# Kernel tuning notes

Hardware: AMD Instinct MI355X
Metric: run time of the kernel (lower is better)

The kernel has to match this reference:

```python
import jax, jax.numpy as jnp
import numpy as np

EMBED_DIM = 128
LAYER_NUM = 5
NUM_GRAPHS = 8192
ATOM_VOCAB = 119
BOND_VOCAB = 8  # get_bond_feature_int_dims()[0] + 3
BN_EPS = 1e-5


def setup_inputs() -> dict:
    key = jax.random.key(0)
    ks = jax.random.split(key, 12)
    N, E, d = 300000, 600000, EMBED_DIM
    x = jax.random.randint(ks[0], (N, 9), 0, ATOM_VOCAB)
    edge_index = jax.random.randint(ks[1], (2, E), 0, N)
    edge_attr = jax.random.randint(ks[2], (E, 3), 0, BOND_VOCAB)
    batch = jnp.sort(jax.random.randint(ks[3], (N,), 0, NUM_GRAPHS))
    s1 = (2.0 / (ATOM_VOCAB + d)) ** 0.5  # xavier-ish scales
    atom_emb = jax.random.normal(ks[4], (ATOM_VOCAB, d), jnp.float32) * s1
    bond_emb = jax.random.normal(ks[5], (BOND_VOCAB, d), jnp.float32) * s1
    L = LAYER_NUM
    W1 = jax.random.normal(ks[6], (L, d, 2 * d), jnp.float32) * (2.0 / (3 * d)) ** 0.5
    b1 = jnp.zeros((L, 2 * d), jnp.float32)
    W2 = jax.random.normal(ks[7], (L, 2 * d, d), jnp.float32) * (2.0 / (3 * d)) ** 0.5
    b2 = jnp.zeros((L, d), jnp.float32)
    gamma = jnp.ones((L, d), jnp.float32)
    beta = jnp.zeros((L, d), jnp.float32)
    return {"x": x, "edge_index": edge_index, "edge_attr": edge_attr, "batch": batch,
            "atom_emb": atom_emb, "bond_emb": bond_emb, "W1": W1, "b1": b1,
            "W2": W2, "b2": b2, "gamma": gamma, "beta": beta}


def reference(x, edge_index, edge_attr, batch, atom_emb, bond_emb, W1, b1, W2, b2, gamma, beta):
    # node / edge embeddings from first integer feature column
    h = atom_emb[x[:, 0]]                      # [N, d]
    e = bond_emb[edge_attr[:, 0]]              # [E, d]
    src, dst = edge_index[0], edge_index[1]
    N = h.shape[0]
    for l in range(LAYER_NUM):
        # GINE message: relu(h_src + edge_attr), scatter-sum to dst
        msg = jax.nn.relu(h[src] + e)                             # [E, d]
        agg = jax.ops.segment_sum(msg, dst, num_segments=N)       # [N, d]
        z = h + agg                                               # (1+eps)*h + agg, eps=0
        # GIN MLP: Linear(d,2d) -> ReLU -> Linear(2d,d)
        z = jax.nn.relu(z @ W1[l] + b1[l]) @ W2[l] + b2[l]
        # BatchNorm1d over nodes (training statistics, biased variance)
        mean = jnp.mean(z, axis=0)
        var = jnp.var(z, axis=0)
        z = (z - mean) * jax.lax.rsqrt(var + BN_EPS) * gamma[l] + beta[l]
        # dropout is identity in eval; relu except on last layer
        h = z if l == LAYER_NUM - 1 else jax.nn.relu(z)
    # global_add_pool
    return jax.ops.segment_sum(h, batch, num_segments=NUM_GRAPHS)  # [G, d]
```

## Files before the change

kernel.cpp:

```cpp
#include <hip/hip_runtime.h>
#include <hip/hip_bf16.h>

#define LAYERS 5
#define STATS_NB 16
#define EMAX 160

typedef __attribute__((ext_vector_type(8))) short short8v;
typedef __attribute__((ext_vector_type(4))) float f32x4;
typedef __attribute__((ext_vector_type(4))) unsigned int u32x4;

#define MFMA(a, b, c) __builtin_amdgcn_mfma_f32_16x16x32_bf16(a, b, c, 0, 0, 0)

__device__ __forceinline__ void atomAddF(float* p, float v) {
    __hip_atomic_fetch_add(p, v, __ATOMIC_RELAXED, __HIP_MEMORY_SCOPE_AGENT);
}

__device__ __forceinline__ float b2f(unsigned short u) { return __uint_as_float(((unsigned)u) << 16); }
__device__ __forceinline__ unsigned short f2b(float f) {
    __hip_bfloat16 h = __float2bfloat16(f);
    unsigned short u;
    __builtin_memcpy(&u, &h, 2);
    return u;
}
__device__ __forceinline__ void st4(unsigned short* p, float4 v) {
    ushort4 u;
    u.x = f2b(v.x); u.y = f2b(v.y); u.z = f2b(v.z); u.w = f2b(v.w);
    *(ushort4*)p = u;
}
__device__ __forceinline__ void unpack8(u32x4 u, float* f) {
#pragma unroll
    for (int k = 0; k < 4; ++k) {
        unsigned int w = u[k];
        f[2 * k]     = __uint_as_float(w << 16);
        f[2 * k + 1] = __uint_as_float(w & 0xffff0000u);
    }
}

__global__ void init_h_kernel(const int* __restrict__ x, const float* __restrict__ atom_emb,
                              unsigned short* __restrict__ h, float* __restrict__ scv,
                              float* __restrict__ shv, int N) {
    if (blockIdx.x == 0 && threadIdx.x < 128) {
        scv[threadIdx.x] = 1.f;
        shv[threadIdx.x] = 0.f;
    }
    int tid = blockIdx.x * blockDim.x + threadIdx.x;
    if (tid >= N * 32) return;
    int i = tid >> 5;
    int c4 = (tid & 31) << 2;
    int a = x[i * 9];
    float4 v = *(const float4*)(atom_emb + a * 128 + c4);
    st4(h + (size_t)i * 128 + c4, v);
}

__global__ void hist_kernel(const int* __restrict__ ei, int* __restrict__ cnt, int E) {
    int e = blockIdx.x * blockDim.x + threadIdx.x;
    if (e < E) atomicAdd(&cnt[ei[E + e]], 1);
}

__global__ void scan_block_sum(const int* __restrict__ cnt, int* __restrict__ bsum, int N) {
    __shared__ int ls[256];
    int base = blockIdx.x * 1024;
    int tid = threadIdx.x;
    int s = 0;
#pragma unroll
    for (int j = 0; j < 4; ++j) {
        int i = base + tid * 4 + j;
        if (i < N) s += cnt[i];
    }
    ls[tid] = s;
    __syncthreads();
    for (int off = 128; off > 0; off >>= 1) {
        if (tid < off) ls[tid] += ls[tid + off];
        __syncthreads();
    }
    if (tid == 0) bsum[blockIdx.x] = ls[0];
}

__global__ void scan_bsums(int* __restrict__ bsum, int nb) {
    if (blockIdx.x == 0 && threadIdx.x == 0) {
        int acc = 0;
        for (int i = 0; i < nb; ++i) { int v = bsum[i]; bsum[i] = acc; acc += v; }
    }
}

__global__ void scan_write(int* __restrict__ cnt_cursor, const int* __restrict__ bsum,
                           int* __restrict__ rowptr, int N, int E) {
    __shared__ int ls[256];
    int base = blockIdx.x * 1024;
    int tid = threadIdx.x;
    int v[4];
    int s = 0;
#pragma unroll
    for (int j = 0; j < 4; ++j) {
        int i = base + tid * 4 + j;
        v[j] = (i < N) ? cnt_cursor[i] : 0;
        s += v[j];
    }
    ls[tid] = s;
    __syncthreads();
    if (tid == 0) {
        int acc = 0;
        for (int i = 0; i < 256; ++i) { int t = ls[i]; ls[i] = acc; acc += t; }
    }
    __syncthreads();
    int off = bsum[blockIdx.x] + ls[tid];
#pragma unroll
    for (int j = 0; j < 4; ++j) {
        int i = base + tid * 4 + j;
        if (i < N) {
            rowptr[i] = off;
            cnt_cursor[i] = off;
            off += v[j];
        }
    }
    if (blockIdx.x == 0 && tid == 0) rowptr[N] = E;
}

__global__ void scatter_kernel(const int* __restrict__ ei, const int* __restrict__ eattr,
                               int* __restrict__ cursor, int* __restrict__ ebuf, int E) {
    int e = blockIdx.x * blockDim.x + threadIdx.x;
    if (e >= E) return;
    int d = ei[E + e];
    int pos = atomicAdd(&cursor[d], 1);
    ebuf[pos] = ei[e] | (eattr[e * 3] << 19);
}

__global__ void pack_w1_kernel(const float* __restrict__ W1,
                               unsigned short* __restrict__ wh, unsigned short* __restrict__ wl) {
    int tid = blockIdx.x * blockDim.x + threadIdx.x;
    if (tid >= LAYERS * 16 * 4 * 64) return;
    int lane = tid & 63;
    int ks = (tid >> 6) & 3;
    int nt = (tid >> 8) & 15;
    int l  = tid >> 12;
    int n  = nt * 16 + (lane & 15);
    int k0 = ks * 32 + ((lane >> 4) << 3);
    unsigned short hh[8], ll[8];
#pragma unroll
    for (int j = 0; j < 8; ++j) {
        float v = W1[((size_t)l * 128 + k0 + j) * 256 + n];
        hh[j] = f2b(v);
        ll[j] = f2b(v - b2f(hh[j]));
    }
    size_t off = (size_t)tid * 8;
    *(ushort4*)(wh + off)     = make_ushort4(hh[0], hh[1], hh[2], hh[3]);
    *(ushort4*)(wh + off + 4) = make_ushort4(hh[4], hh[5], hh[6], hh[7]);
    *(ushort4*)(wl + off)     = make_ushort4(ll[0], ll[1], ll[2], ll[3]);
    *(ushort4*)(wl + off + 4) = make_ushort4(ll[4], ll[5], ll[6], ll[7]);
}

__global__ void pack_w2_kernel(const float* __restrict__ W2,
                               unsigned short* __restrict__ wh, unsigned short* __restrict__ wl) {
    int tid = blockIdx.x * blockDim.x + threadIdx.x;
    if (tid >= LAYERS * 8 * 8 * 64) return;
    int lane = tid & 63;
    int ks = (tid >> 6) & 7;
    int nt = (tid >> 9) & 7;
    int l  = tid >> 12;
    int n  = nt * 16 + (lane & 15);
    int k0 = ks * 32 + ((lane >> 4) << 3);
    unsigned short hh[8], ll[8];
#pragma unroll
    for (int j = 0; j < 8; ++j) {
        float v = W2[((size_t)l * 256 + k0 + j) * 128 + n];
        hh[j] = f2b(v);
        ll[j] = f2b(v - b2f(hh[j]));
    }
    size_t off = (size_t)tid * 8;
    *(ushort4*)(wh + off)     = make_ushort4(hh[0], hh[1], hh[2], hh[3]);
    *(ushort4*)(wh + off + 4) = make_ushort4(hh[4], hh[5], hh[6], hh[7]);
    *(ushort4*)(wl + off)     = make_ushort4(ll[0], ll[1], ll[2], ll[3]);
    *(ushort4*)(wl + off + 4) = make_ushort4(ll[4], ll[5], ll[6], ll[7]);
}

__global__ __launch_bounds__(512, 6) void fused_mlp_kernel(
        const unsigned short* __restrict__ zin,
        const int* __restrict__ rowptr, const int* __restrict__ ebuf,
        const float* __restrict__ bond_emb,
        const float* __restrict__ scv, const float* __restrict__ shv, float clampv,
        const unsigned short* __restrict__ w1h, const unsigned short* __restrict__ w1l,
        const unsigned short* __restrict__ w2h, const unsigned short* __restrict__ w2l,
        const float* __restrict__ b1, const float* __restrict__ b2,
        unsigned short* __restrict__ zout, float* __restrict__ stats_part, int N) {
    __shared__ float bemb[8 * 128];
    __shared__ float scl[128], shl[128];
    __shared__ int els[EMAX];
    __shared__ int rp[65];
    __shared__ unsigned short xs[64][136];
    __shared__ unsigned short ts[64][136];

    int tid = threadIdx.x;
    int rowBase = blockIdx.x * 64;
    int lane = tid & 63;
    int wv = tid >> 6;

    for (int i = tid; i < 1024; i += 512) bemb[i] = bond_emb[i];
    if (tid < 128) { scl[tid] = scv[tid]; shl[tid] = shv[tid]; }
    if (tid >= 128 && tid <= 192) {
        int t = tid - 128;
        int rr = rowBase + t;
        rp[t] = rowptr[rr < N ? rr : N];
    }
    __syncthreads();
    int beg = rp[0];
    int cnt = rp[64] - beg;
    for (int i = tid; i < cnt && i < EMAX; i += 512) els[i] = ebuf[beg + i];
    __syncthreads();

    {
        int r = tid >> 3;
        int c0 = (tid & 7) << 4;
        int row = rowBase + r;
        float xv[16];
        if (row < N) {
            const unsigned short* hp = zin + (size_t)row * 128 + c0;
            u32x4 u0 = *(const u32x4*)hp;
            u32x4 u1 = *(const u32x4*)(hp + 8);
            float rv[16];
            unpack8(u0, rv);
            unpack8(u1, rv + 8);
#pragma unroll
            for (int i2 = 0; i2 < 16; ++i2)
                xv[i2] = fmaxf(fmaf(rv[i2], scl[c0 + i2], shl[c0 + i2]), clampv);
            int rb = rp[r] - beg;
            int re = rp[r + 1] - beg;
            const float* bemb_c = bemb + c0;
            for (int j = rb; j < re; ++j) {
                int ee = (j < EMAX) ? els[j] : ebuf[beg + j];
                int src = ee & 0x7FFFF;
                int b = ee >> 19;
                const unsigned short* sp = zin + (size_t)src * 128 + c0;
                u32x4 s0 = *(const u32x4*)sp;
                u32x4 s1 = *(const u32x4*)(sp + 8);
                float sv[16];
                unpack8(s0, sv);
                unpack8(s1, sv + 8);
                const float* bp = bemb_c + b * 128;
#pragma unroll
                for (int i2 = 0; i2 < 16; ++i2) {
                    float hv = fmaxf(fmaf(sv[i2], scl[c0 + i2], shl[c0 + i2]), clampv);
                    xv[i2] += fmaxf(hv + bp[i2], 0.f);
                }
            }
        } else {
#pragma unroll
            for (int i2 = 0; i2 < 16; ++i2) xv[i2] = 0.f;
        }
#pragma unroll
        for (int k = 0; k < 4; ++k) {
            *(ushort4*)(&xs[r][c0 + k * 4]) = make_ushort4(
                f2b(xv[k * 4 + 0]), f2b(xv[k * 4 + 1]), f2b(xv[k * 4 + 2]), f2b(xv[k * 4 + 3]));
        }
    }
    __syncthreads();

    int lrow = lane & 15;
    int lk8 = (lane >> 4) << 3;
    int rgrp = (lane >> 4) << 2;
    int wm = wv >> 2;
    int wn = wv & 3;

    f32x4 acc2[2][2];
#pragma unroll
    for (int mt = 0; mt < 2; ++mt)
#pragma unroll
        for (int t = 0; t < 2; ++t) acc2[mt][t] = (f32x4){0.f, 0.f, 0.f, 0.f};

#pragma unroll
    for (int half = 0; half < 2; ++half) {
        f32x4 acc1[2][2];
#pragma unroll
        for (int mt = 0; mt < 2; ++mt)
#pragma unroll
            for (int t = 0; t < 2; ++t) acc1[mt][t] = (f32x4){0.f, 0.f, 0.f, 0.f};

#pragma unroll
        for (int ks = 0; ks < 4; ++ks) {
            int kb = ks * 32 + lk8;
            short8v ah[2];
#pragma unroll
            for (int mt = 0; mt < 2; ++mt) {
                int mrow = (wm * 2 + mt) * 16 + lrow;
                ah[mt] = *(const short8v*)(&xs[mrow][kb]);
            }
#pragma unroll
            for (int t = 0; t < 2; ++t) {
                int nt = half * 8 + wn * 2 + t;
                size_t off = ((size_t)(nt * 4 + ks) * 64 + lane) * 8;
                short8v wh = *(const short8v*)(w1h + off);
                short8v wl = *(const short8v*)(w1l + off);
#pragma unroll
                for (int mt = 0; mt < 2; ++mt) {
                    acc1[mt][t] = MFMA(ah[mt], wl, acc1[mt][t]);
                    acc1[mt][t] = MFMA(ah[mt], wh, acc1[mt][t]);
                }
            }
        }

        if (half) __syncthreads();

#pragma unroll
        for (int t = 0; t < 2; ++t) {
            int coll = (wn * 2 + t) * 16 + lrow;
            float bb = b1[half * 128 + coll];
#pragma unroll
            for (int mt = 0; mt < 2; ++mt) {
                int row0 = (wm * 2 + mt) * 16 + rgrp;
#pragma unroll
                for (int r = 0; r < 4; ++r) {
                    ts[row0 + r][coll] = f2b(fmaxf(acc1[mt][t][r] + bb, 0.f));
                }
            }
        }
        __syncthreads();

#pragma unroll
        for (int ksl = 0; ksl < 4; ++ksl) {
            int kb = ksl * 32 + lk8;
            short8v ah[2];
#pragma unroll
            for (int mt = 0; mt < 2; ++mt) {
                int mrow = (wm * 2 + mt) * 16 + lrow;
                ah[mt] = *(const short8v*)(&ts[mrow][kb]);
            }
#pragma unroll
            for (int t = 0; t < 2; ++t) {
                int nt = wn * 2 + t;
                int ks = half * 4 + ksl;
                size_t off = ((size_t)(nt * 8 + ks) * 64 + lane) * 8;
                short8v wh = *(const short8v*)(w2h + off);
                short8v wl = *(const short8v*)(w2l + off);
#pragma unroll
                for (int mt = 0; mt < 2; ++mt) {
                    acc2[mt][t] = MFMA(ah[mt], wl, acc2[mt][t]);
                    acc2[mt][t] = MFMA(ah[mt], wh, acc2[mt][t]);
                }
            }
        }
    }

#pragma unroll
    for (int t = 0; t < 2; ++t) {
        int col = (wn * 2 + t) * 16 + lrow;
        float bb = b2[col];
        float s = 0.f, q = 0.f;
#pragma unroll
        for (int mt = 0; mt < 2; ++mt) {
#pragma unroll
            for (int r = 0; r < 4; ++r) {
                int row = rowBase + (wm * 2 + mt) * 16 + rgrp + r;
                if (row < N) {
                    float zv = acc2[mt][t][r] + bb;
                    zout[(size_t)row * 128 + col] = f2b(zv);
                    s += zv;
                    q += zv * zv;
                }
            }
        }
        s += __shfl_xor(s, 16, 64);
        s += __shfl_xor(s, 32, 64);
        q += __shfl_xor(q, 16, 64);
        q += __shfl_xor(q, 32, 64);
        if (lane < 16) {
            float* sp = stats_part + (size_t)(blockIdx.x & (STATS_NB - 1)) * 256;
            atomAddF(sp + col, s);
            atomAddF(sp + 128 + col, q);
        }
    }
}

__global__ void reduce_stats_sc_kernel(float* __restrict__ part,
                                       const float* __restrict__ gamma, const float* __restrict__ beta,
                                       float* __restrict__ scv, float* __restrict__ shv, float invN) {
    __shared__ float ls[256];
    int c = threadIdx.x;
    float s = 0.f;
    for (int i = 0; i < STATS_NB; ++i) {
        s += part[i * 256 + c];
        part[i * 256 + c] = 0.f;
    }
    ls[c] = s;
    __syncthreads();
    if (c < 128) {
        float mean = ls[c] * invN;
        float var = ls[128 + c] * invN - mean * mean;
        float sc = rsqrtf(var + 1e-5f) * gamma[c];
        scv[c] = sc;
        shv[c] = beta[c] - mean * sc;
    }
}

__global__ __launch_bounds__(256) void pool_seg_kernel(const unsigned short* __restrict__ zb,
                                                       const int* __restrict__ batch,
                                                       const float* __restrict__ scv,
                                                       const float* __restrict__ shv,
                                                       float* __restrict__ out, int N, int G) {
    int g = blockIdx.x * 4 + (threadIdx.x >> 6);
    if (g >= G) return;
    int lane = threadIdx.x & 63;
    int lo = 0, hi = N;
    while (lo < hi) { int m = (lo + hi) >> 1; if (batch[m] < g) lo = m + 1; else hi = m; }
    int s = lo;
    hi = N;
    while (lo < hi) { int m = (lo + hi) >> 1; if (batch[m] < g + 1) lo = m + 1; else hi = m; }
    int e = lo;
    int c2 = lane * 2;
    float a0 = 0.f, a1 = 0.f;
    for (int i = s; i < e; ++i) {
        ushort2 u = *(const ushort2*)(zb + (size_t)i * 128 + c2);
        a0 += b2f(u.x);
        a1 += b2f(u.y);
    }
    float cntf = (float)(e - s);
    float o0 = scv[c2] * a0 + cntf * shv[c2];
    float o1 = scv[c2 + 1] * a1 + cntf * shv[c2 + 1];
    *(float2*)(out + (size_t)g * 128 + c2) = make_float2(o0, o1);
}

extern "C" void kernel_launch(void* const* d_in, const int* in_sizes, int n_in,
                              void* d_out, int out_size, void* d_ws, size_t ws_size,
                              hipStream_t stream) {
    const int* x        = (const int*)d_in[0];
    const int* ei       = (const int*)d_in[1];
    const int* eattr    = (const int*)d_in[2];
    const int* batch    = (const int*)d_in[3];
    const float* atom_e = (const float*)d_in[4];
    const float* bond_e = (const float*)d_in[5];
    const float* W1     = (const float*)d_in[6];
    const float* b1     = (const float*)d_in[7];
    const float* W2     = (const float*)d_in[8];
    const float* b2     = (const float*)d_in[9];
    const float* gamma  = (const float*)d_in[10];
    const float* beta   = (const float*)d_in[11];

    int N = in_sizes[0] / 9;
    int E = in_sizes[1] / 2;
    int G = out_size / 128;

    auto align = [](size_t v) { return (v + 255) & ~(size_t)255; };
    char* ws = (char*)d_ws;
    unsigned short* bufA = (unsigned short*)ws; ws += align((size_t)N * 128 * 2);
    unsigned short* bufB = (unsigned short*)ws; ws += align((size_t)N * 128 * 2);
    int* rowptr  = (int*)ws;                 ws += align((size_t)(N + 1) * 4);
    int* cursor  = (int*)ws;                 ws += align((size_t)N * 4);
    int* ebuf    = (int*)ws;                 ws += align((size_t)E * 4);
    int* bsum    = (int*)ws;                 ws += align((size_t)4096 * 4);
    unsigned short* w1h = (unsigned short*)ws; ws += align((size_t)LAYERS * 32768 * 2);
    unsigned short* w1l = (unsigned short*)ws; ws += align((size_t)LAYERS * 32768 * 2);
    unsigned short* w2h = (unsigned short*)ws; ws += align((size_t)LAYERS * 32768 * 2);
    unsigned short* w2l = (unsigned short*)ws; ws += align((size_t)LAYERS * 32768 * 2);
    float* stats_part = (float*)ws;          ws += align((size_t)STATS_NB * 256 * 4);
    float* scv = (float*)ws;                 ws += align(128 * 4);
    float* shv = (float*)ws;

    float invN = 1.0f / (float)N;
    int nf4 = N * 32;
    int nb = (N + 1023) / 1024;

    init_h_kernel<<<(nf4 + 255) / 256, 256, 0, stream>>>(x, atom_e, bufA, scv, shv, N);

    hipMemsetAsync(cursor, 0, (size_t)N * 4, stream);
    hist_kernel<<<(E + 255) / 256, 256, 0, stream>>>(ei, cursor, E);
    scan_block_sum<<<nb, 256, 0, stream>>>(cursor, bsum, N);
    scan_bsums<<<1, 64, 0, stream>>>(bsum, nb);
    scan_write<<<nb, 256, 0, stream>>>(cursor, bsum, rowptr, N, E);
    scatter_kernel<<<(E + 255) / 256, 256, 0, stream>>>(ei, eattr, cursor, ebuf, E);

    pack_w1_kernel<<<(LAYERS * 16 * 4 * 64 + 255) / 256, 256, 0, stream>>>(W1, w1h, w1l);
    pack_w2_kernel<<<(LAYERS * 8 * 8 * 64 + 255) / 256, 256, 0, stream>>>(W2, w2h, w2l);
    hipMemsetAsync(stats_part, 0, (size_t)STATS_NB * 256 * 4, stream);

    unsigned short* zin = bufA;
    unsigned short* zout = bufB;
    for (int l = 0; l < LAYERS; ++l) {
        float clampv = (l == 0) ? -3.0e38f : 0.0f;
        fused_mlp_kernel<<<(N + 63) / 64, 512, 0, stream>>>(
            zin, rowptr, ebuf, bond_e, scv, shv, clampv,
            w1h + (size_t)l * 32768, w1l + (size_t)l * 32768,
            w2h + (size_t)l * 32768, w2l + (size_t)l * 32768,
            b1 + (size_t)l * 256, b2 + (size_t)l * 128,
            zout, stats_part, N);
        reduce_stats_sc_kernel<<<1, 256, 0, stream>>>(stats_part, gamma + (size_t)l * 128,
                                                      beta + (size_t)l * 128, scv, shv, invN);
        unsigned short* tmp = zin; zin = zout; zout = tmp;
    }

    pool_seg_kernel<<<(G + 3) / 4, 256, 0, stream>>>(zin, batch, scv, shv, (float*)d_out, N, G);
}
```

Baseline: 866.7 us.

## Switch MLP to 32x32 MFMA tiles and fold BN stats reduction into consumers

Replaces the 16x16x32 bf16 MFMA tiling with 32x32x16 MFMAs, with each wave computing a single 32x32 tile. The weight packing kernels are rewritten to the new fragment layout. The separate single-block reduce_stats kernel is removed: each layer's kernel and the pool kernel now sum the previous layer's partial statistics and compute scale/shift themselves, using per-layer stats buffers that are zeroed once. This removes five tiny serial launches at the cost of redundant per-block reduction work and a different MFMA register and LDS access pattern.

```diff
diff --git a/kernel.cpp b/kernel.cpp
--- a/kernel.cpp
+++ b/kernel.cpp
@@ -6,10 +6,10 @@
 #define EMAX 160
 
 typedef __attribute__((ext_vector_type(8))) short short8v;
-typedef __attribute__((ext_vector_type(4))) float f32x4;
+typedef __attribute__((ext_vector_type(16))) float f32x16;
 typedef __attribute__((ext_vector_type(4))) unsigned int u32x4;
 
-#define MFMA(a, b, c) __builtin_amdgcn_mfma_f32_16x16x32_bf16(a, b, c, 0, 0, 0)
+#define MFMA32(a, b, c) __builtin_amdgcn_mfma_f32_32x32x16_bf16(a, b, c, 0, 0, 0)
 
 __device__ __forceinline__ void atomAddF(float* p, float v) {
     __hip_atomic_fetch_add(p, v, __ATOMIC_RELAXED, __HIP_MEMORY_SCOPE_AGENT);
@@ -37,12 +37,7 @@
 }
 
 __global__ void init_h_kernel(const int* __restrict__ x, const float* __restrict__ atom_emb,
-                              unsigned short* __restrict__ h, float* __restrict__ scv,
-                              float* __restrict__ shv, int N) {
-    if (blockIdx.x == 0 && threadIdx.x < 128) {
-        scv[threadIdx.x] = 1.f;
-        shv[threadIdx.x] = 0.f;
-    }
+                              unsigned short* __restrict__ h, int N) {
     int tid = blockIdx.x * blockDim.x + threadIdx.x;
     if (tid >= N * 32) return;
     int i = tid >> 5;
@@ -128,13 +123,13 @@
 __global__ void pack_w1_kernel(const float* __restrict__ W1,
                                unsigned short* __restrict__ wh, unsigned short* __restrict__ wl) {
     int tid = blockIdx.x * blockDim.x + threadIdx.x;
-    if (tid >= LAYERS * 16 * 4 * 64) return;
+    if (tid >= LAYERS * 8 * 8 * 64) return;
     int lane = tid & 63;
-    int ks = (tid >> 6) & 3;
-    int nt = (tid >> 8) & 15;
+    int ks = (tid >> 6) & 7;
+    int nt = (tid >> 9) & 7;
     int l  = tid >> 12;
-    int n  = nt * 16 + (lane & 15);
-    int k0 = ks * 32 + ((lane >> 4) << 3);
+    int n  = nt * 32 + (lane & 31);
+    int k0 = ks * 16 + ((lane >> 5) << 3);
     unsigned short hh[8], ll[8];
 #pragma unroll
     for (int j = 0; j < 8; ++j) {
@@ -152,13 +147,13 @@
 __global__ void pack_w2_kernel(const float* __restrict__ W2,
                                unsigned short* __restrict__ wh, unsigned short* __restrict__ wl) {
     int tid = blockIdx.x * blockDim.x + threadIdx.x;
-    if (tid >= LAYERS * 8 * 8 * 64) return;
+    if (tid >= LAYERS * 4 * 16 * 64) return;
     int lane = tid & 63;
-    int ks = (tid >> 6) & 7;
-    int nt = (tid >> 9) & 7;
+    int ks = (tid >> 6) & 15;
+    int nt = (tid >> 10) & 3;
     int l  = tid >> 12;
-    int n  = nt * 16 + (lane & 15);
-    int k0 = ks * 32 + ((lane >> 4) << 3);
+    int n  = nt * 32 + (lane & 31);
+    int k0 = ks * 16 + ((lane >> 5) << 3);
     unsigned short hh[8], ll[8];
 #pragma unroll
     for (int j = 0; j < 8; ++j) {
@@ -173,15 +168,18 @@
     *(ushort4*)(wl + off + 4) = make_ushort4(ll[4], ll[5], ll[6], ll[7]);
 }
 
+template <bool FIRST>
 __global__ __launch_bounds__(512, 6) void fused_mlp_kernel(
         const unsigned short* __restrict__ zin,
         const int* __restrict__ rowptr, const int* __restrict__ ebuf,
         const float* __restrict__ bond_emb,
-        const float* __restrict__ scv, const float* __restrict__ shv, float clampv,
+        const float* __restrict__ stats_prev,
+        const float* __restrict__ gamma_prev, const float* __restrict__ beta_prev,
+        float invN, float clampv,
         const unsigned short* __restrict__ w1h, const unsigned short* __restrict__ w1l,
         const unsigned short* __restrict__ w2h, const unsigned short* __restrict__ w2l,
         const float* __restrict__ b1, const float* __restrict__ b2,
-        unsigned short* __restrict__ zout, float* __restrict__ stats_part, int N) {
+        unsigned short* __restrict__ zout, float* __restrict__ stats_out, int N) {
     __shared__ float bemb[8 * 128];
     __shared__ float scl[128], shl[128];
     __shared__ int els[EMAX];
@@ -195,9 +193,18 @@
     int wv = tid >> 6;
 
     for (int i = tid; i < 1024; i += 512) bemb[i] = bond_emb[i];
-    if (tid < 128) { scl[tid] = scv[tid]; shl[tid] = shv[tid]; }
-    if (tid >= 128 && tid <= 192) {
-        int t = tid - 128;
+    if (FIRST) {
+        if (tid < 128) { scl[tid] = 1.f; shl[tid] = 0.f; }
+    } else {
+        if (tid < 256) {
+            float s = 0.f;
+#pragma unroll
+            for (int i = 0; i < STATS_NB; ++i) s += stats_prev[i * 256 + tid];
+            if (tid < 128) scl[tid] = s; else shl[tid - 128] = s;
+        }
+    }
+    if (tid >= 256 && tid <= 320) {
+        int t = tid - 256;
         int rr = rowBase + t;
         rp[t] = rowptr[rr < N ? rr : N];
     }
@@ -205,6 +212,14 @@
     int beg = rp[0];
     int cnt = rp[64] - beg;
     for (int i = tid; i < cnt && i < EMAX; i += 512) els[i] = ebuf[beg + i];
+    if (!FIRST && tid < 128) {
+        float S = scl[tid], Q = shl[tid];
+        float mean = S * invN;
+        float var = Q * invN - mean * mean;
+        float sc = rsqrtf(var + 1e-5f) * gamma_prev[tid];
+        scl[tid] = sc;
+        shl[tid] = beta_prev[tid] - mean * sc;
+    }
     __syncthreads();
 
     {
@@ -254,150 +269,109 @@
     }
     __syncthreads();
 
-    int lrow = lane & 15;
-    int lk8 = (lane >> 4) << 3;
-    int rgrp = (lane >> 4) << 2;
+    int lane31 = lane & 31;
+    int lk8 = (lane >> 5) << 3;
     int wm = wv >> 2;
     int wn = wv & 3;
-
-    f32x4 acc2[2][2];
-#pragma unroll
-    for (int mt = 0; mt < 2; ++mt)
-#pragma unroll
-        for (int t = 0; t < 2; ++t) acc2[mt][t] = (f32x4){0.f, 0.f, 0.f, 0.f};
+    int coll = wn * 32 + lane31;
+
+    f32x16 acc2;
+#pragma unroll
+    for (int r = 0; r < 16; ++r) acc2[r] = 0.f;
 
 #pragma unroll
     for (int half = 0; half < 2; ++half) {
-        f32x4 acc1[2][2];
-#pragma unroll
-        for (int mt = 0; mt < 2; ++mt)
-#pragma unroll
-            for (int t = 0; t < 2; ++t) acc1[mt][t] = (f32x4){0.f, 0.f, 0.f, 0.f};
-
-#pragma unroll
-        for (int ks = 0; ks < 4; ++ks) {
-            int kb = ks * 32 + lk8;
-            short8v ah[2];
-#pragma unroll
-            for (int mt = 0; mt < 2; ++mt) {
-                int mrow = (wm * 2 + mt) * 16 + lrow;
-                ah[mt] = *(const short8v*)(&xs[mrow][kb]);
+        f32x16 acc1;
+#pragma unroll
+        for (int r = 0; r < 16; ++r) acc1[r] = 0.f;
+
+#pragma unroll
+        for (int ks = 0; ks < 8; ++ks) {
+            short8v ah = *(const short8v*)(&xs[wm * 32 + lane31][ks * 16 + lk8]);
+            int ntg = half * 4 + wn;
+            size_t off = ((size_t)(ntg * 8 + ks) * 64 + lane) * 8;
+            short8v wwh = *(const short8v*)(w1h + off);
+            short8v wwl = *(const short8v*)(w1l + off);
+            acc1 = MFMA32(ah, wwl, acc1);
+            acc1 = MFMA32(ah, wwh, acc1);
+        }
+
+        if (half) __syncthreads();
+
+        {
+            float bb = b1[half * 128 + coll];
+#pragma unroll
+            for (int reg = 0; reg < 16; ++reg) {
+                int rrow = wm * 32 + (reg & 3) + 8 * (reg >> 2) + 4 * (lane >> 5);
+                ts[rrow][coll] = f2b(fmaxf(acc1[reg] + bb, 0.f));
             }
-#pragma unroll
-            for (int t = 0; t < 2; ++t) {
-                int nt = half * 8 + wn * 2 + t;
-                size_t off = ((size_t)(nt * 4 + ks) * 64 + lane) * 8;
-                short8v wh = *(const short8v*)(w1h + off);
-                short8v wl = *(const short8v*)(w1l + off);
-#pragma unroll
-                for (int mt = 0; mt < 2; ++mt) {
-                    acc1[mt][t] = MFMA(ah[mt], wl, acc1[mt][t]);
-                    acc1[mt][t] = MFMA(ah[mt], wh, acc1[mt][t]);
-                }
+        }
+        __syncthreads();
+
+#pragma unroll
+        for (int ksl = 0; ksl < 8; ++ksl) {
+            short8v ah = *(const short8v*)(&ts[wm * 32 + lane31][ksl * 16 + lk8]);
+            int ks2 = half * 8 + ksl;
+            size_t off = ((size_t)(wn * 16 + ks2) * 64 + lane) * 8;
+            short8v wwh = *(const short8v*)(w2h + off);
+            short8v wwl = *(const short8v*)(w2l + off);
+            acc2 = MFMA32(ah, wwl, acc2);
+            acc2 = MFMA32(ah, wwh, acc2);
+        }
+    }
+
+    {
+        float bb = b2[coll];
+        float s = 0.f, q = 0.f;
+#pragma unroll
+        for (int reg = 0; reg < 16; ++reg) {
+            int row = rowBase + wm * 32 + (reg & 3) + 8 * (reg >> 2) + 4 * (lane >> 5);
+            if (row < N) {
+                float zv = acc2[reg] + bb;
+                zout[(size_t)row * 128 + coll] = f2b(zv);
+                s += zv;
+                q += zv * zv;
             }
         }
-
-        if (half) __syncthreads();
-
-#pragma unroll
-        for (int t = 0; t < 2; ++t) {
-            int coll = (wn * 2 + t) * 16 + lrow;
-            float bb = b1[half * 128 + coll];
-#pragma unroll
-            for (int mt = 0; mt < 2; ++mt) {
-                int row0 = (wm * 2 + mt) * 16 + rgrp;
-#pragma unroll
-                for (int r = 0; r < 4; ++r) {
-                    ts[row0 + r][coll] = f2b(fmaxf(acc1[mt][t][r] + bb, 0.f));
-                }
-            }
-        }
-        __syncthreads();
-
-#pragma unroll
-        for (int ksl = 0; ksl < 4; ++ksl) {
-            int kb = ksl * 32 + lk8;
-            short8v ah[2];
-#pragma unroll
-            for (int mt = 0; mt < 2; ++mt) {
-                int mrow = (wm * 2 + mt) * 16 + lrow;
-                ah[mt] = *(const short8v*)(&ts[mrow][kb]);
-            }
-#pragma unroll
-            for (int t = 0; t < 2; ++t) {
-                int nt = wn * 2 + t;
-                int ks = half * 4 + ksl;
-                size_t off = ((size_t)(nt * 8 + ks) * 64 + lane) * 8;
-                short8v wh = *(const short8v*)(w2h + off);
-                short8v wl = *(const short8v*)(w2l + off);
-#pragma unroll
-                for (int mt = 0; mt < 2; ++mt) {
-                    acc2[mt][t] = MFMA(ah[mt], wl, acc2[mt][t]);
-                    acc2[mt][t] = MFMA(ah[mt], wh, acc2[mt][t]);
-                }
-            }
-        }
-    }
-
-#pragma unroll
-    for (int t = 0; t < 2; ++t) {
-        int col = (wn * 2 + t) * 16 + lrow;
-        float bb = b2[col];
-        float s = 0.f, q = 0.f;
-#pragma unroll
-        for (int mt = 0; mt < 2; ++mt) {
-#pragma unroll
-            for (int r = 0; r < 4; ++r) {
-                int row = rowBase + (wm * 2 + mt) * 16 + rgrp + r;
-                if (row < N) {
-                    float zv = acc2[mt][t][r] + bb;
-                    zout[(size_t)row * 128 + col] = f2b(zv);
-                    s += zv;
-                    q += zv * zv;
-                }
-            }
-        }
-        s += __shfl_xor(s, 16, 64);
         s += __shfl_xor(s, 32, 64);
-        q += __shfl_xor(q, 16, 64);
         q += __shfl_xor(q, 32, 64);
-        if (lane < 16) {
-            float* sp = stats_part + (size_t)(blockIdx.x & (STATS_NB - 1)) * 256;
-            atomAddF(sp + col, s);
-            atomAddF(sp + 128 + col, q);
-        }
-    }
-}
-
-__global__ void reduce_stats_sc_kernel(float* __restrict__ part,
-                                       const float* __restrict__ gamma, const float* __restrict__ beta,
-                                       float* __restrict__ scv, float* __restrict__ shv, float invN) {
-    __shared__ float ls[256];
-    int c = threadIdx.x;
-    float s = 0.f;
-    for (int i = 0; i < STATS_NB; ++i) {
-        s += part[i * 256 + c];
-        part[i * 256 + c] = 0.f;
-    }
-    ls[c] = s;
-    __syncthreads();
-    if (c < 128) {
-        float mean = ls[c] * invN;
-        float var = ls[128 + c] * invN - mean * mean;
-        float sc = rsqrtf(var + 1e-5f) * gamma[c];
-        scv[c] = sc;
-        shv[c] = beta[c] - mean * sc;
+        if (lane < 32) {
+            float* sp = stats_out + (size_t)(blockIdx.x & (STATS_NB - 1)) * 256;
+            atomAddF(sp + coll, s);
+            atomAddF(sp + 128 + coll, q);
+        }
     }
 }
 
 __global__ __launch_bounds__(256) void pool_seg_kernel(const unsigned short* __restrict__ zb,
                                                        const int* __restrict__ batch,
-                                                       const float* __restrict__ scv,
-                                                       const float* __restrict__ shv,
-                                                       float* __restrict__ out, int N, int G) {
-    int g = blockIdx.x * 4 + (threadIdx.x >> 6);
+                                                       const float* __restrict__ stats4,
+                                                       const float* __restrict__ gamma4,
+                                                       const float* __restrict__ beta4,
+                                                       float* __restrict__ out, int N, int G,
+                                                       float invN) {
+    __shared__ float sums[256];
+    __shared__ float scp[128], shp[128];
+    int tid = threadIdx.x;
+    {
+        float s = 0.f;
+#pragma unroll
+        for (int i = 0; i < STATS_NB; ++i) s += stats4[i * 256 + tid];
+        sums[tid] = s;
+    }
+    __syncthreads();
+    if (tid < 128) {
+        float mean = sums[tid] * invN;
+        float var = sums[128 + tid] * invN - mean * mean;
+        float sc = rsqrtf(var + 1e-5f) * gamma4[tid];
+        scp[tid] = sc;
+        shp[tid] = beta4[tid] - mean * sc;
+    }
+    __syncthreads();
+
+    int g = blockIdx.x * 4 + (tid >> 6);
     if (g >= G) return;
-    int lane = threadIdx.x & 63;
+    int lane = tid & 63;
     int lo = 0, hi = N;
     while (lo < hi) { int m = (lo + hi) >> 1; if (batch[m] < g) lo = m + 1; else hi = m; }
     int s = lo;
@@ -412,8 +386,8 @@
         a1 += b2f(u.y);
     }
     float cntf = (float)(e - s);
-    float o0 = scv[c2] * a0 + cntf * shv[c2];
-    float o1 = scv[c2 + 1] * a1 + cntf * shv[c2 + 1];
+    float o0 = scp[c2] * a0 + cntf * shp[c2];
+    float o1 = scp[c2 + 1] * a1 + cntf * shp[c2 + 1];
     *(float2*)(out + (size_t)g * 128 + c2) = make_float2(o0, o1);
 }
 
@@ -449,15 +423,13 @@
     unsigned short* w1l = (unsigned short*)ws; ws += align((size_t)LAYERS * 32768 * 2);
     unsigned short* w2h = (unsigned short*)ws; ws += align((size_t)LAYERS * 32768 * 2);
     unsigned short* w2l = (unsigned short*)ws; ws += align((size_t)LAYERS * 32768 * 2);
-    float* stats_part = (float*)ws;          ws += align((size_t)STATS_NB * 256 * 4);
-    float* scv = (float*)ws;                 ws += align(128 * 4);
-    float* shv = (float*)ws;
+    float* stats = (float*)ws;               ws += align((size_t)LAYERS * STATS_NB * 256 * 4);
 
     float invN = 1.0f / (float)N;
     int nf4 = N * 32;
     int nb = (N + 1023) / 1024;
 
-    init_h_kernel<<<(nf4 + 255) / 256, 256, 0, stream>>>(x, atom_e, bufA, scv, shv, N);
+    init_h_kernel<<<(nf4 + 255) / 256, 256, 0, stream>>>(x, atom_e, bufA, N);
 
     hipMemsetAsync(cursor, 0, (size_t)N * 4, stream);
     hist_kernel<<<(E + 255) / 256, 256, 0, stream>>>(ei, cursor, E);
@@ -466,24 +438,37 @@
     scan_write<<<nb, 256, 0, stream>>>(cursor, bsum, rowptr, N, E);
     scatter_kernel<<<(E + 255) / 256, 256, 0, stream>>>(ei, eattr, cursor, ebuf, E);
 
-    pack_w1_kernel<<<(LAYERS * 16 * 4 * 64 + 255) / 256, 256, 0, stream>>>(W1, w1h, w1l);
-    pack_w2_kernel<<<(LAYERS * 8 * 8 * 64 + 255) / 256, 256, 0, stream>>>(W2, w2h, w2l);
-    hipMemsetAsync(stats_part, 0, (size_t)STATS_NB * 256 * 4, stream);
+    pack_w1_kernel<<<(LAYERS * 4096 + 255) / 256, 256, 0, stream>>>(W1, w1h, w1l);
+    pack_w2_kernel<<<(LAYERS * 4096 + 255) / 256, 256, 0, stream>>>(W2, w2h, w2l);
+    hipMemsetAsync(stats, 0, (size_t)LAYERS * STATS_NB * 256 * 4, stream);
 
     unsigned short* zin = bufA;
     unsigned short* zout = bufB;
     for (int l = 0; l < LAYERS; ++l) {
         float clampv = (l == 0) ? -3.0e38f : 0.0f;
-        fused_mlp_kernel<<<(N + 63) / 64, 512, 0, stream>>>(
-            zin, rowptr, ebuf, bond_e, scv, shv, clampv,
-            w1h + (size_t)l * 32768, w1l + (size_t)l * 32768,
-            w2h + (size_t)l * 32768, w2l + (size_t)l * 32768,
-            b1 + (size_t)l * 256, b2 + (size_t)l * 128,
-            zout, stats_part, N);
-        reduce_stats_sc_kernel<<<1, 256, 0, stream>>>(stats_part, gamma + (size_t)l * 128,
-                                                      beta + (size_t)l * 128, scv, shv, invN);
+        float* st_prev = stats + (size_t)(l - 1) * STATS_NB * 256;
+        float* st_out  = stats + (size_t)l * STATS_NB * 256;
+        if (l == 0) {
+            fused_mlp_kernel<true><<<(N + 63) / 64, 512, 0, stream>>>(
+                zin, rowptr, ebuf, bond_e, nullptr, gamma, beta, invN, clampv,
+                w1h + (size_t)l * 32768, w1l + (size_t)l * 32768,
+                w2h + (size_t)l * 32768, w2l + (size_t)l * 32768,
+                b1 + (size_t)l * 256, b2 + (size_t)l * 128,
+                zout, st_out, N);
+        } else {
+            fused_mlp_kernel<false><<<(N + 63) / 64, 512, 0, stream>>>(
+                zin, rowptr, ebuf, bond_e, st_prev,
+                gamma + (size_t)(l - 1) * 128, beta + (size_t)(l - 1) * 128, invN, clampv,
+                w1h + (size_t)l * 32768, w1l + (size_t)l * 32768,
+                w2h + (size_t)l * 32768, w2l + (size_t)l * 32768,
+                b1 + (size_t)l * 256, b2 + (size_t)l * 128,
+                zout, st_out, N);
+        }
         unsigned short* tmp = zin; zin = zout; zout = tmp;
     }
 
-    pool_seg_kernel<<<(G + 3) / 4, 256, 0, stream>>>(zin, batch, scv, shv, (float*)d_out, N, G);
-}
+    pool_seg_kernel<<<(G + 3) / 4, 256, 0, stream>>>(
+        zin, batch, stats + (size_t)(LAYERS - 1) * STATS_NB * 256,
+        gamma + (size_t)(LAYERS - 1) * 128, beta + (size_t)(LAYERS - 1) * 128,
+        (float*)d_out, N, G, invN);
+}
```

Measured after the change: 883.2 us. Within noise of the previous version (+1.9%).
